# Kernel tuning notes

Measured on AMD Instinct MI355X. Metric: run time of the kernel, lower is better.

## Reference

```python
import jax, jax.numpy as jnp
import numpy as np

N_NODES = 100000
N_EDGES = 1600000
D_IN = 256
D_OUT = 256


def setup_inputs() -> dict:
    key = jax.random.key(0)
    k1, k2, k3, k4, k5 = jax.random.split(key, 5)
    x = jax.random.normal(k1, (N_NODES, D_IN), dtype=jnp.float32)
    edge_src = jax.random.randint(k2, (N_EDGES,), 0, N_NODES, dtype=jnp.int32)
    edge_dst = jax.random.randint(k3, (N_EDGES,), 0, N_NODES, dtype=jnp.int32)
    edge_val = jax.random.uniform(k4, (N_EDGES,), dtype=jnp.float32)
    stdv = 1.0 / np.sqrt(D_OUT)
    weight = jax.random.uniform(k5, (D_IN, D_OUT), dtype=jnp.float32,
                                minval=-stdv, maxval=stdv)
    return {"x": x, "edge_src": edge_src, "edge_dst": edge_dst,
            "edge_val": edge_val, "weight": weight}


def reference(x, edge_src, edge_dst, edge_val, weight):
    # torch.spmm(adj, x): out[dst] += adj_val * x[src]
    msgs = x[edge_src] * edge_val[:, None]                     # [E, D_IN]
    agg = jax.ops.segment_sum(msgs, edge_dst,
                              num_segments=x.shape[0])         # [N, D_IN]
    # torch.mm(aggregated, weight)
    return agg @ weight                                        # [N, D_OUT]
```

## Files before the change

### kernel.cpp

```cpp
#include <hip/hip_runtime.h>
#include <hip/hip_bf16.h>

#define D 256
#define BDST 128
#define CAP 3072
#define TILE 6144

typedef __attribute__((ext_vector_type(8))) short short8;
typedef __attribute__((ext_vector_type(4))) float f32x4;

static __device__ __forceinline__ unsigned short f2bf(float f) {
    union { float f; unsigned u; } u; u.f = f;
    unsigned r = u.u + 0x7FFF + ((u.u >> 16) & 1);
    return (unsigned short)(r >> 16);
}

static __device__ __forceinline__ float bf2f(unsigned short b) {
    union { unsigned u; float f; } u; u.u = ((unsigned)b) << 16;
    return u.f;
}

static __device__ __forceinline__ unsigned cvtpk(float a, float b) {
    unsigned r;
    asm("v_cvt_pk_bf16_f32 %0, %1, %2" : "=v"(r) : "v"(a), "v"(b));
    return r;
}

__global__ __launch_bounds__(64) void build_wf_kernel(
    const float* __restrict__ W, unsigned short* __restrict__ wF) {
    int fid = blockIdx.x;
    int kt = fid >> 4, nt = fid & 15;
    int lane = threadIdx.x;
    int col = nt * 16 + (lane & 15);
    int k0 = kt * 32 + (lane >> 4) * 8;
    unsigned short frag[8];
#pragma unroll
    for (int j = 0; j < 8; ++j) frag[j] = f2bf(W[(k0 + j) * D + col]);
    *(short8*)(wF + ((size_t)fid * 64 + lane) * 8) = *(short8*)frag;
}

__global__ __launch_bounds__(256) void gemm_kernel(
    const float* __restrict__ x, const unsigned short* __restrict__ wF,
    unsigned short* __restrict__ y, int n_nodes) {
    const int lane = threadIdx.x & 63;
    const int wave = threadIdx.x >> 6;
    const int rsel = lane & 15;
    const int koff = (lane >> 4) * 8;
    const int row0 = blockIdx.x * 64 + wave * 16;
    if (row0 >= n_nodes) return;

    int row = row0 + rsel;
    int rowc = row < n_nodes ? row : n_nodes - 1;
    const float* xp = x + (size_t)rowc * D + koff;

    short8 a[8];
#pragma unroll
    for (int kt = 0; kt < 8; ++kt) {
        f32x4 lo = *(const f32x4*)(xp + kt * 32);
        f32x4 hi = *(const f32x4*)(xp + kt * 32 + 4);
        union { unsigned u[4]; short8 s; } pk;
        pk.u[0] = cvtpk(lo[0], lo[1]);
        pk.u[1] = cvtpk(lo[2], lo[3]);
        pk.u[2] = cvtpk(hi[0], hi[1]);
        pk.u[3] = cvtpk(hi[2], hi[3]);
        a[kt] = pk.s;
    }

    f32x4 acc[16];
#pragma unroll
    for (int nt = 0; nt < 16; ++nt) acc[nt] = (f32x4){0.f, 0.f, 0.f, 0.f};

    const short8* wf = (const short8*)wF;
#pragma unroll
    for (int kt = 0; kt < 8; ++kt) {
#pragma unroll
        for (int nt = 0; nt < 16; ++nt) {
            short8 b = wf[(kt * 16 + nt) * 64 + lane];
            acc[nt] = __builtin_amdgcn_mfma_f32_16x16x32_bf16(a[kt], b, acc[nt], 0, 0, 0);
        }
    }

    int crow0 = row0 + (lane >> 4) * 4;
#pragma unroll
    for (int nt = 0; nt < 16; ++nt) {
        int ccol = nt * 16 + rsel;
#pragma unroll
        for (int i = 0; i < 4; ++i) {
            int r = crow0 + i;
            if (r < n_nodes) y[(size_t)r * D + ccol] = f2bf(acc[nt][i]);
        }
    }
}

__global__ __launch_bounds__(256) void hist_bucket_kernel(
    const int* __restrict__ edst, int* __restrict__ gcount,
    int n_edges, int nb) {
    __shared__ int h[1024];
    for (int j = threadIdx.x; j < nb; j += 256) h[j] = 0;
    __syncthreads();
    int i = blockIdx.x * 256 + threadIdx.x;
    int stride = gridDim.x * 256;
    for (; i < n_edges; i += stride) atomicAdd(&h[edst[i] >> 7], 1);
    __syncthreads();
    for (int j = threadIdx.x; j < nb; j += 256) {
        int v = h[j];
        if (v) atomicAdd(&gcount[j], v);
    }
}

__global__ __launch_bounds__(1024) void scan_bucket_kernel(
    const int* __restrict__ gcount, int* __restrict__ offs,
    int* __restrict__ cursor, int nb) {
    __shared__ int t[1024];
    int tid = threadIdx.x;
    int c = (tid < nb) ? gcount[tid] : 0;
    t[tid] = c;
    __syncthreads();
    for (int off = 1; off < 1024; off <<= 1) {
        int v = (tid >= off) ? t[tid - off] : 0;
        __syncthreads();
        t[tid] += v;
        __syncthreads();
    }
    if (tid < nb) { int e = t[tid] - c; offs[tid] = e; cursor[tid] = e; }
}

__global__ __launch_bounds__(1024) void fill_ms_kernel(
    const int* __restrict__ esrc, const int* __restrict__ edst,
    const float* __restrict__ eval, int* __restrict__ cursor,
    int2* __restrict__ binned, int n_edges, int nb) {
    __shared__ int lhist[1024];
    __shared__ int lscan[1024];
    __shared__ int lbase[1024];
    __shared__ int lcur[1024];

    int tid = threadIdx.x;
    int tb = blockIdx.x * TILE;
    int m = n_edges - tb; if (m > TILE) m = TILE;

    int src[6], dst[6]; float val[6];
#pragma unroll
    for (int j = 0; j < 6; ++j) {
        int i = tid + j * 1024;
        if (i < m) { src[j] = esrc[tb + i]; dst[j] = edst[tb + i]; val[j] = eval[tb + i]; }
    }

    for (int j = tid; j < nb; j += 1024) lhist[j] = 0;
    __syncthreads();
#pragma unroll
    for (int j = 0; j < 6; ++j)
        if (tid + j * 1024 < m) atomicAdd(&lhist[dst[j] >> 7], 1);
    __syncthreads();

    int c = (tid < nb) ? lhist[tid] : 0;
    lscan[tid] = c;
    __syncthreads();
    for (int off = 1; off < 1024; off <<= 1) {
        int v = (tid >= off) ? lscan[tid - off] : 0;
        __syncthreads();
        lscan[tid] += v;
        __syncthreads();
    }
    if (tid < nb) {
        int lofs = lscan[tid] - c;
        int gbase = c ? atomicAdd(&cursor[tid], c) : 0;
        lbase[tid] = gbase - lofs;
        lcur[tid] = lofs;
    }
    __syncthreads();

#pragma unroll
    for (int j = 0; j < 6; ++j) {
        if (tid + j * 1024 < m) {
            int d = dst[j];
            int b = d >> 7;
            int pos = atomicAdd(&lcur[b], 1);
            binned[lbase[b] + pos] =
                make_int2(src[j] | ((d & (BDST - 1)) << 20), __float_as_int(val[j]));
        }
    }
}

__global__ __launch_bounds__(512) void bucket_gather_kernel(
    const unsigned short* __restrict__ y, const int* __restrict__ offs,
    const int* __restrict__ bend, const int2* __restrict__ binned,
    float* __restrict__ out, int n_nodes) {
    __shared__ int2 lcsr[CAP];
    __shared__ int lhist[BDST];
    __shared__ int lscan[BDST];
    __shared__ int lofs[BDST];
    __shared__ int lcur[BDST];

    int b = blockIdx.x;
    int tid = threadIdx.x;
    int beg = offs[b];
    int end = bend[b];
    int cnt = end - beg;
    int nch = cnt > 0 ? (cnt + CAP - 1) / CAP : 1;

    const int hw = tid >> 5;
    const int lane = tid & 31;
    const unsigned short* yl = y + lane * 8;

    for (int c = 0; c < nch; ++c) {
        int cb = beg + c * CAP;
        int ce = cb + CAP < end ? cb + CAP : end;
        int m = ce > cb ? ce - cb : 0;

        int2 ec[6];
#pragma unroll
        for (int j = 0; j < 6; ++j) {
            int i = tid + j * 512;
            if (i < m) ec[j] = binned[cb + i];
        }

        for (int j = tid; j < BDST; j += 512) lhist[j] = 0;
        __syncthreads();
#pragma unroll
        for (int j = 0; j < 6; ++j)
            if (tid + j * 512 < m) atomicAdd(&lhist[(ec[j].x >> 20) & (BDST - 1)], 1);
        __syncthreads();
        if (tid < BDST) lscan[tid] = lhist[tid];
        __syncthreads();
        for (int off = 1; off < BDST; off <<= 1) {
            int v = 0;
            if (tid < BDST && tid >= off) v = lscan[tid - off];
            __syncthreads();
            if (tid < BDST) lscan[tid] += v;
            __syncthreads();
        }
        if (tid < BDST) {
            int e = lscan[tid] - lhist[tid];
            lofs[tid] = e;
            lcur[tid] = e;
        }
        __syncthreads();
#pragma unroll
        for (int j = 0; j < 6; ++j) {
            if (tid + j * 512 < m) {
                int pos = atomicAdd(&lcur[(ec[j].x >> 20) & (BDST - 1)], 1);
                lcsr[pos] = ec[j];
            }
        }
        __syncthreads();

        for (int dl = hw; dl < BDST; dl += 16) {
            int d = b * BDST + dl;
            if (d >= n_nodes) break;
            int i0 = lofs[dl];
            int i1 = lcur[dl];
            float acc[8] = {0.f, 0.f, 0.f, 0.f, 0.f, 0.f, 0.f, 0.f};
            int i = i0;
            for (; i + 4 <= i1; i += 4) {
                int2 e0 = lcsr[i];
                int2 e1 = lcsr[i + 1];
                int2 e2 = lcsr[i + 2];
                int2 e3 = lcsr[i + 3];
                short8 r0 = *(const short8*)(yl + (size_t)(e0.x & 0xFFFFF) * D);
                short8 r1 = *(const short8*)(yl + (size_t)(e1.x & 0xFFFFF) * D);
                short8 r2 = *(const short8*)(yl + (size_t)(e2.x & 0xFFFFF) * D);
                short8 r3 = *(const short8*)(yl + (size_t)(e3.x & 0xFFFFF) * D);
                float v0 = __int_as_float(e0.y), v1 = __int_as_float(e1.y);
                float v2 = __int_as_float(e2.y), v3 = __int_as_float(e3.y);
#pragma unroll
                for (int j = 0; j < 8; ++j) {
                    acc[j] += v0 * bf2f((unsigned short)r0[j]);
                    acc[j] += v1 * bf2f((unsigned short)r1[j]);
                    acc[j] += v2 * bf2f((unsigned short)r2[j]);
                    acc[j] += v3 * bf2f((unsigned short)r3[j]);
                }
            }
            for (; i < i1; ++i) {
                int2 e0 = lcsr[i];
                float v0 = __int_as_float(e0.y);
                short8 r0 = *(const short8*)(yl + (size_t)(e0.x & 0xFFFFF) * D);
#pragma unroll
                for (int j = 0; j < 8; ++j) acc[j] += v0 * bf2f((unsigned short)r0[j]);
            }
            float* op = out + (size_t)d * D + lane * 8;
            if (c == 0) {
                *(f32x4*)(op)     = (f32x4){acc[0], acc[1], acc[2], acc[3]};
                *(f32x4*)(op + 4) = (f32x4){acc[4], acc[5], acc[6], acc[7]};
            } else {
                f32x4 o0 = *(f32x4*)(op);
                f32x4 o1 = *(f32x4*)(op + 4);
                o0[0] += acc[0]; o0[1] += acc[1]; o0[2] += acc[2]; o0[3] += acc[3];
                o1[0] += acc[4]; o1[1] += acc[5]; o1[2] += acc[6]; o1[3] += acc[7];
                *(f32x4*)(op)     = o0;
                *(f32x4*)(op + 4) = o1;
            }
        }
        __syncthreads();
    }
}

extern "C" void kernel_launch(void* const* d_in, const int* in_sizes, int n_in,
                              void* d_out, int out_size, void* d_ws, size_t ws_size,
                              hipStream_t stream) {
    const float* x    = (const float*)d_in[0];
    const int*   esrc = (const int*)d_in[1];
    const int*   edst = (const int*)d_in[2];
    const float* eval = (const float*)d_in[3];
    const float* W    = (const float*)d_in[4];
    float* out = (float*)d_out;

    const int n_nodes = in_sizes[0] / D;
    const int n_edges = in_sizes[1];
    const int nb = (n_nodes + BDST - 1) / BDST;

    char* ws = (char*)d_ws;
    unsigned short* y  = (unsigned short*)ws;  ws += (size_t)n_nodes * D * 2;
    unsigned short* wF = (unsigned short*)ws;  ws += (size_t)D * D * 2;
    int*  gcount  = (int*)ws;                  ws += 4096;
    int*  offs    = (int*)ws;                  ws += 4096;
    int*  cursor  = (int*)ws;                  ws += 4096;
    int2* binned  = (int2*)ws;                 ws += (size_t)n_edges * 8;

    hipMemsetAsync(gcount, 0, (size_t)nb * sizeof(int), stream);

    build_wf_kernel<<<128, 64, 0, stream>>>(W, wF);
    gemm_kernel<<<(n_nodes + 63) / 64, 256, 0, stream>>>(x, wF, y, n_nodes);

    hist_bucket_kernel<<<256, 256, 0, stream>>>(edst, gcount, n_edges, nb);
    scan_bucket_kernel<<<1, 1024, 0, stream>>>(gcount, offs, cursor, nb);

    const int ntiles = (n_edges + TILE - 1) / TILE;
    fill_ms_kernel<<<ntiles, 1024, 0, stream>>>(esrc, edst, eval, cursor, binned, n_edges, nb);

    bucket_gather_kernel<<<nb, 512, 0, stream>>>(y, offs, cursor, binned, out, n_nodes);
}
```

Baseline: 244.5 us.

## Fuse W-prep with histogram, stage GEMM output via LDS, shrink gather blocks

```diff
diff --git a/kernel.cpp b/kernel.cpp
--- a/kernel.cpp
+++ b/kernel.cpp
@@ -3,8 +3,9 @@
 
 #define D 256
 #define BDST 128
-#define CAP 3072
+#define CAP 2560
 #define TILE 6144
+#define YROW 264
 
 typedef __attribute__((ext_vector_type(8))) short short8;
 typedef __attribute__((ext_vector_type(4))) float f32x4;
@@ -26,30 +27,122 @@
     return r;
 }
 
-__global__ __launch_bounds__(64) void build_wf_kernel(
-    const float* __restrict__ W, unsigned short* __restrict__ wF) {
-    int fid = blockIdx.x;
-    int kt = fid >> 4, nt = fid & 15;
-    int lane = threadIdx.x;
-    int col = nt * 16 + (lane & 15);
-    int k0 = kt * 32 + (lane >> 4) * 8;
-    unsigned short frag[8];
-#pragma unroll
-    for (int j = 0; j < 8; ++j) frag[j] = f2bf(W[(k0 + j) * D + col]);
-    *(short8*)(wF + ((size_t)fid * 64 + lane) * 8) = *(short8*)frag;
+__global__ __launch_bounds__(256) void prep_kernel(
+    const float* __restrict__ W, unsigned short* __restrict__ wF,
+    const int* __restrict__ edst, int* __restrict__ gcount,
+    int n_edges, int nb) {
+    int tid = threadIdx.x;
+    if (blockIdx.x < 32) {
+        int fid = blockIdx.x * 4 + (tid >> 6);
+        int lane = tid & 63;
+        int kt = fid >> 4, nt = fid & 15;
+        int col = nt * 16 + (lane & 15);
+        int k0 = kt * 32 + (lane >> 4) * 8;
+        unsigned short frag[8];
+#pragma unroll
+        for (int j = 0; j < 8; ++j) frag[j] = f2bf(W[(k0 + j) * D + col]);
+        *(short8*)(wF + ((size_t)fid * 64 + lane) * 8) = *(short8*)frag;
+    } else {
+        __shared__ int h[1024];
+        for (int j = tid; j < nb; j += 256) h[j] = 0;
+        __syncthreads();
+        int i = (blockIdx.x - 32) * 256 + tid;
+        int stride = (gridDim.x - 32) * 256;
+        for (; i < n_edges; i += stride) atomicAdd(&h[edst[i] >> 7], 1);
+        __syncthreads();
+        for (int j = tid; j < nb; j += 256) {
+            int v = h[j];
+            if (v) atomicAdd(&gcount[j], v);
+        }
+    }
+}
+
+__global__ __launch_bounds__(1024) void scan_bucket_kernel(
+    const int* __restrict__ gcount, int* __restrict__ offs,
+    int* __restrict__ cursor, int nb) {
+    __shared__ int t[1024];
+    int tid = threadIdx.x;
+    int c = (tid < nb) ? gcount[tid] : 0;
+    t[tid] = c;
+    __syncthreads();
+    for (int off = 1; off < 1024; off <<= 1) {
+        int v = (tid >= off) ? t[tid - off] : 0;
+        __syncthreads();
+        t[tid] += v;
+        __syncthreads();
+    }
+    if (tid < nb) { int e = t[tid] - c; offs[tid] = e; cursor[tid] = e; }
+}
+
+__global__ __launch_bounds__(1024) void fill_ms_kernel(
+    const int* __restrict__ esrc, const int* __restrict__ edst,
+    const float* __restrict__ eval, int* __restrict__ cursor,
+    int2* __restrict__ binned, int n_edges, int nb) {
+    __shared__ int lhist[1024];
+    __shared__ int lscan[1024];
+    __shared__ int lbase[1024];
+    __shared__ int lcur[1024];
+
+    int tid = threadIdx.x;
+    int tb = blockIdx.x * TILE;
+    int m = n_edges - tb; if (m > TILE) m = TILE;
+
+    int src[6], dst[6]; float val[6];
+#pragma unroll
+    for (int j = 0; j < 6; ++j) {
+        int i = tid + j * 1024;
+        if (i < m) { src[j] = esrc[tb + i]; dst[j] = edst[tb + i]; val[j] = eval[tb + i]; }
+    }
+
+    for (int j = tid; j < nb; j += 1024) lhist[j] = 0;
+    __syncthreads();
+#pragma unroll
+    for (int j = 0; j < 6; ++j)
+        if (tid + j * 1024 < m) atomicAdd(&lhist[dst[j] >> 7], 1);
+    __syncthreads();
+
+    int c = (tid < nb) ? lhist[tid] : 0;
+    lscan[tid] = c;
+    __syncthreads();
+    for (int off = 1; off < 1024; off <<= 1) {
+        int v = (tid >= off) ? lscan[tid - off] : 0;
+        __syncthreads();
+        lscan[tid] += v;
+        __syncthreads();
+    }
+    if (tid < nb) {
+        int lofs = lscan[tid] - c;
+        int gbase = c ? atomicAdd(&cursor[tid], c) : 0;
+        lbase[tid] = gbase - lofs;
+        lcur[tid] = lofs;
+    }
+    __syncthreads();
+
+#pragma unroll
+    for (int j = 0; j < 6; ++j) {
+        if (tid + j * 1024 < m) {
+            int d = dst[j];
+            int b = d >> 7;
+            int pos = atomicAdd(&lcur[b], 1);
+            binned[lbase[b] + pos] =
+                make_int2(src[j] | ((d & (BDST - 1)) << 20), __float_as_int(val[j]));
+        }
+    }
 }
 
 __global__ __launch_bounds__(256) void gemm_kernel(
     const float* __restrict__ x, const unsigned short* __restrict__ wF,
     unsigned short* __restrict__ y, int n_nodes) {
-    const int lane = threadIdx.x & 63;
-    const int wave = threadIdx.x >> 6;
+    __shared__ unsigned short ytile[64 * YROW];
+
+    const int tid  = threadIdx.x;
+    const int lane = tid & 63;
+    const int wave = tid >> 6;
     const int rsel = lane & 15;
     const int koff = (lane >> 4) * 8;
-    const int row0 = blockIdx.x * 64 + wave * 16;
-    if (row0 >= n_nodes) return;
-
-    int row = row0 + rsel;
+    const int brow = blockIdx.x * 64;
+
+    int row = brow + wave * 16 + rsel;
     int rowc = row < n_nodes ? row : n_nodes - 1;
     const float* xp = x + (size_t)rowc * D + koff;
 
@@ -80,108 +173,27 @@
         }
     }
 
-    int crow0 = row0 + (lane >> 4) * 4;
+    int lrow0 = wave * 16 + (lane >> 4) * 4;
 #pragma unroll
     for (int nt = 0; nt < 16; ++nt) {
         int ccol = nt * 16 + rsel;
 #pragma unroll
-        for (int i = 0; i < 4; ++i) {
-            int r = crow0 + i;
-            if (r < n_nodes) y[(size_t)r * D + ccol] = f2bf(acc[nt][i]);
-        }
-    }
-}
-
-__global__ __launch_bounds__(256) void hist_bucket_kernel(
-    const int* __restrict__ edst, int* __restrict__ gcount,
-    int n_edges, int nb) {
-    __shared__ int h[1024];
-    for (int j = threadIdx.x; j < nb; j += 256) h[j] = 0;
-    __syncthreads();
-    int i = blockIdx.x * 256 + threadIdx.x;
-    int stride = gridDim.x * 256;
-    for (; i < n_edges; i += stride) atomicAdd(&h[edst[i] >> 7], 1);
-    __syncthreads();
-    for (int j = threadIdx.x; j < nb; j += 256) {
-        int v = h[j];
-        if (v) atomicAdd(&gcount[j], v);
-    }
-}
-
-__global__ __launch_bounds__(1024) void scan_bucket_kernel(
-    const int* __restrict__ gcount, int* __restrict__ offs,
-    int* __restrict__ cursor, int nb) {
-    __shared__ int t[1024];
-    int tid = threadIdx.x;
-    int c = (tid < nb) ? gcount[tid] : 0;
-    t[tid] = c;
-    __syncthreads();
-    for (int off = 1; off < 1024; off <<= 1) {
-        int v = (tid >= off) ? t[tid - off] : 0;
-        __syncthreads();
-        t[tid] += v;
-        __syncthreads();
-    }
-    if (tid < nb) { int e = t[tid] - c; offs[tid] = e; cursor[tid] = e; }
-}
-
-__global__ __launch_bounds__(1024) void fill_ms_kernel(
-    const int* __restrict__ esrc, const int* __restrict__ edst,
-    const float* __restrict__ eval, int* __restrict__ cursor,
-    int2* __restrict__ binned, int n_edges, int nb) {
-    __shared__ int lhist[1024];
-    __shared__ int lscan[1024];
-    __shared__ int lbase[1024];
-    __shared__ int lcur[1024];
-
-    int tid = threadIdx.x;
-    int tb = blockIdx.x * TILE;
-    int m = n_edges - tb; if (m > TILE) m = TILE;
-
-    int src[6], dst[6]; float val[6];
-#pragma unroll
-    for (int j = 0; j < 6; ++j) {
-        int i = tid + j * 1024;
-        if (i < m) { src[j] = esrc[tb + i]; dst[j] = edst[tb + i]; val[j] = eval[tb + i]; }
-    }
-
-    for (int j = tid; j < nb; j += 1024) lhist[j] = 0;
-    __syncthreads();
-#pragma unroll
-    for (int j = 0; j < 6; ++j)
-        if (tid + j * 1024 < m) atomicAdd(&lhist[dst[j] >> 7], 1);
-    __syncthreads();
-
-    int c = (tid < nb) ? lhist[tid] : 0;
-    lscan[tid] = c;
-    __syncthreads();
-    for (int off = 1; off < 1024; off <<= 1) {
-        int v = (tid >= off) ? lscan[tid - off] : 0;
-        __syncthreads();
-        lscan[tid] += v;
-        __syncthreads();
-    }
-    if (tid < nb) {
-        int lofs = lscan[tid] - c;
-        int gbase = c ? atomicAdd(&cursor[tid], c) : 0;
-        lbase[tid] = gbase - lofs;
-        lcur[tid] = lofs;
-    }
-    __syncthreads();
-
-#pragma unroll
-    for (int j = 0; j < 6; ++j) {
-        if (tid + j * 1024 < m) {
-            int d = dst[j];
-            int b = d >> 7;
-            int pos = atomicAdd(&lcur[b], 1);
-            binned[lbase[b] + pos] =
-                make_int2(src[j] | ((d & (BDST - 1)) << 20), __float_as_int(val[j]));
-        }
-    }
-}
-
-__global__ __launch_bounds__(512) void bucket_gather_kernel(
+        for (int i = 0; i < 4; ++i)
+            ytile[(lrow0 + i) * YROW + ccol] = f2bf(acc[nt][i]);
+    }
+    __syncthreads();
+
+#pragma unroll
+    for (int it = 0; it < 8; ++it) {
+        int r = it * 8 + (tid >> 5);
+        int col = (tid & 31) * 8;
+        int gr = brow + r;
+        if (gr < n_nodes)
+            *(short8*)(y + (size_t)gr * D + col) = *(const short8*)(&ytile[r * YROW + col]);
+    }
+}
+
+__global__ __launch_bounds__(256) void bucket_gather_kernel(
     const unsigned short* __restrict__ y, const int* __restrict__ offs,
     const int* __restrict__ bend, const int2* __restrict__ binned,
     float* __restrict__ out, int n_nodes) {
@@ -207,18 +219,18 @@
         int ce = cb + CAP < end ? cb + CAP : end;
         int m = ce > cb ? ce - cb : 0;
 
-        int2 ec[6];
-#pragma unroll
-        for (int j = 0; j < 6; ++j) {
-            int i = tid + j * 512;
+        int2 ec[10];
+#pragma unroll
+        for (int j = 0; j < 10; ++j) {
+            int i = tid + j * 256;
             if (i < m) ec[j] = binned[cb + i];
         }
 
-        for (int j = tid; j < BDST; j += 512) lhist[j] = 0;
-        __syncthreads();
-#pragma unroll
-        for (int j = 0; j < 6; ++j)
-            if (tid + j * 512 < m) atomicAdd(&lhist[(ec[j].x >> 20) & (BDST - 1)], 1);
+        if (tid < BDST) lhist[tid] = 0;
+        __syncthreads();
+#pragma unroll
+        for (int j = 0; j < 10; ++j)
+            if (tid + j * 256 < m) atomicAdd(&lhist[(ec[j].x >> 20) & (BDST - 1)], 1);
         __syncthreads();
         if (tid < BDST) lscan[tid] = lhist[tid];
         __syncthreads();
@@ -236,15 +248,15 @@
         }
         __syncthreads();
 #pragma unroll
-        for (int j = 0; j < 6; ++j) {
-            if (tid + j * 512 < m) {
+        for (int j = 0; j < 10; ++j) {
+            if (tid + j * 256 < m) {
                 int pos = atomicAdd(&lcur[(ec[j].x >> 20) & (BDST - 1)], 1);
                 lcsr[pos] = ec[j];
             }
         }
         __syncthreads();
 
-        for (int dl = hw; dl < BDST; dl += 16) {
+        for (int dl = hw; dl < BDST; dl += 8) {
             int d = b * BDST + dl;
             if (d >= n_nodes) break;
             int i0 = lofs[dl];
@@ -318,14 +330,14 @@
 
     hipMemsetAsync(gcount, 0, (size_t)nb * sizeof(int), stream);
 
-    build_wf_kernel<<<128, 64, 0, stream>>>(W, wF);
-    gemm_kernel<<<(n_nodes + 63) / 64, 256, 0, stream>>>(x, wF, y, n_nodes);
-
-    hist_bucket_kernel<<<256, 256, 0, stream>>>(edst, gcount, n_edges, nb);
+    prep_kernel<<<256, 256, 0, stream>>>(W, wF, edst, gcount, n_edges, nb);
+
     scan_bucket_kernel<<<1, 1024, 0, stream>>>(gcount, offs, cursor, nb);
 
     const int ntiles = (n_edges + TILE - 1) / TILE;
     fill_ms_kernel<<<ntiles, 1024, 0, stream>>>(esrc, edst, eval, cursor, binned, n_edges, nb);
 
-    bucket_gather_kernel<<<nb, 512, 0, stream>>>(y, offs, cursor, binned, out, n_nodes);
-}
+    gemm_kernel<<<(n_nodes + 63) / 64, 256, 0, stream>>>(x, wF, y, n_nodes);
+
+    bucket_gather_kernel<<<nb, 256, 0, stream>>>(y, offs, cursor, binned, out, n_nodes);
+}
```

New measurement: 242.9 us. No clear change (-0.7%).
